# Performance work log

Hardware: AMD Instinct MI355X
Metric: run time of the kernel (lower is better)

The kernel has to match this reference:

```python
import jax, jax.numpy as jnp
import numpy as np

CAP = 512  # per-expert capacity; mean tokens/expert = 4096*4/64 = 256, CAP = mean + ~16 sigma (no drops for seed 0)


def _moe_forward(hidden_states, gate_w, w13, w2, top_k):
    T, H = hidden_states.shape
    E = gate_w.shape[0]
    # --- gating: softmax over expert logits, then top-k (npu_moe_gating_top_k_softmax) ---
    logits = hidden_states @ gate_w.T                      # [T, E]
    probs = jax.nn.softmax(logits, axis=-1)
    topk_w, topk_idx = jax.lax.top_k(probs, top_k)         # [T, K]
    # norm_topk_prob=True and top_k > 1
    topk_w = topk_w / (topk_w.sum(axis=-1, keepdims=True) + 1e-20)
    # --- init_routing: compute each (token, slot)'s rank within its expert ---
    N = T * top_k
    flat_e = topk_idx.reshape(N)                           # [N] expert id per expanded row
    order = jnp.argsort(flat_e)                            # stable sort by expert
    sorted_e = flat_e[order]
    counts = jax.ops.segment_sum(jnp.ones((N,), jnp.int32), flat_e, num_segments=E)
    starts = jnp.cumsum(counts) - counts                   # [E] start offset of each expert group
    rank_sorted = jnp.arange(N, dtype=jnp.int32) - starts[sorted_e].astype(jnp.int32)
    rank = jnp.zeros((N,), jnp.int32).at[order].set(rank_sorted)  # within-expert position
    # --- dispatch into [E, CAP, H] buffers (token gather/scatter) ---
    x_rep = jnp.repeat(hidden_states, top_k, axis=0)       # [N, H]
    disp = jnp.zeros((E, CAP, H), hidden_states.dtype).at[flat_e, rank].set(x_rep)
    # --- grouped GEMM: SwiGLU expert FFN as batched matmuls ---
    h = jnp.einsum('ech,ehf->ecf', disp, w13)              # [E, CAP, 2I]
    g, u = jnp.split(h, 2, axis=-1)
    a = jax.nn.silu(g) * u                                 # [E, CAP, I]
    y = jnp.einsum('eci,eih->ech', a, w2)                  # [E, CAP, H]
    # --- finalize_routing: gather back and weighted combine ---
    out_rows = y[flat_e, rank]                             # [N, H]
    out = (out_rows.reshape(T, top_k, H) * topk_w[..., None]).sum(axis=1)
    return out


def setup_inputs() -> dict:
    key = jax.random.key(0)
    k1, k2, k3, k4 = jax.random.split(key, 4)
    T, H, E, I = 4096, 2048, 64, 768
    hidden_states = jax.random.normal(k1, (T, H), dtype=jnp.float32)
    gate_w = jax.random.normal(k2, (E, H), dtype=jnp.float32) * 0.02
    w13 = jax.random.normal(k3, (E, H, 2 * I), dtype=jnp.float32) * 0.02
    w2 = jax.random.normal(k4, (E, I, H), dtype=jnp.float32) * 0.02
    return {"hidden_states": hidden_states, "gate_w": gate_w, "w13": w13, "w2": w2, "top_k": 4}


def reference(hidden_states, gate_w, w13, w2, top_k):
    return _moe_forward(hidden_states, gate_w, w13, w2, top_k)
```

## Files before the change

### kernel.cpp

```cpp
#include <hip/hip_runtime.h>
#include <hip/hip_bf16.h>

#define T_TOK 4096
#define HDIM  2048
#define NEXP  64
#define IDIM  768
#define TOPK  4
#define CAPE  512
#define NFLAT (T_TOK*TOPK)

typedef __bf16        bf16x8 __attribute__((ext_vector_type(8)));
typedef float         f32x4  __attribute__((ext_vector_type(4)));
typedef unsigned int  u32x4  __attribute__((ext_vector_type(4)));

__device__ __forceinline__ unsigned short f2bf(float f) {
  __bf16 b = (__bf16)f;
  return __builtin_bit_cast(unsigned short, b);
}
__device__ __forceinline__ unsigned pack2(float lo, float hi) {
  return (unsigned)f2bf(lo) | ((unsigned)f2bf(hi) << 16);
}
__device__ __forceinline__ int fswz(int row) { return ((row & 7) ^ ((row >> 3) & 7)) & 7; }
__device__ __forceinline__ int swz(int row, int chunk) {
  return row*128 + (((chunk ^ fswz(row)) & 7) << 4);
}
__device__ __forceinline__ void gload_lds16(const void* g, void* l) {
  __builtin_amdgcn_global_load_lds(
      (const __attribute__((address_space(1))) unsigned int*)g,
      (__attribute__((address_space(3))) unsigned int*)l, 16, 0, 0);
}

__global__ __launch_bounds__(256) void k_gating(
    const float* __restrict__ hs, const float* __restrict__ gw,
    unsigned short* __restrict__ hs_bf, int* __restrict__ tidx, float* __restrict__ tw)
{
  __shared__ float lg[16][64];
  const int tid = threadIdx.x;
  const int t0  = blockIdx.x * 16;

  {
    const f32x4* src = (const f32x4*)(hs + (size_t)t0 * HDIM);
    for (int i = tid; i < 16 * HDIM / 4; i += 256) {
      f32x4 v = src[i];
      ushort4 o;
      o.x = f2bf(v[0]); o.y = f2bf(v[1]); o.z = f2bf(v[2]); o.w = f2bf(v[3]);
      *(ushort4*)(hs_bf + (size_t)t0 * HDIM + (size_t)i * 4) = o;
    }
  }

  const int lane = tid & 63, wv = tid >> 6;
  {
    const f32x4* gr = (const f32x4*)(gw + (size_t)lane * HDIM);
    const f32x4* x0 = (const f32x4*)(hs + (size_t)(t0 + wv*4 + 0) * HDIM);
    const f32x4* x1 = (const f32x4*)(hs + (size_t)(t0 + wv*4 + 1) * HDIM);
    const f32x4* x2 = (const f32x4*)(hs + (size_t)(t0 + wv*4 + 2) * HDIM);
    const f32x4* x3 = (const f32x4*)(hs + (size_t)(t0 + wv*4 + 3) * HDIM);
    float a0=0.f, a1=0.f, a2=0.f, a3=0.f;
    for (int h = 0; h < HDIM/4; ++h) {
      f32x4 g = gr[h];
      f32x4 v0 = x0[h], v1 = x1[h], v2 = x2[h], v3 = x3[h];
      a0 += g[0]*v0[0] + g[1]*v0[1] + g[2]*v0[2] + g[3]*v0[3];
      a1 += g[0]*v1[0] + g[1]*v1[1] + g[2]*v1[2] + g[3]*v1[3];
      a2 += g[0]*v2[0] + g[1]*v2[1] + g[2]*v2[2] + g[3]*v2[3];
      a3 += g[0]*v3[0] + g[1]*v3[1] + g[2]*v3[2] + g[3]*v3[3];
    }
    lg[wv*4+0][lane] = a0;
    lg[wv*4+1][lane] = a1;
    lg[wv*4+2][lane] = a2;
    lg[wv*4+3][lane] = a3;
  }
  __syncthreads();

  if (tid < 16) {
    const int t = t0 + tid;
    unsigned long long chosen = 0ull;
    float bv[4]; int bi[4];
#pragma unroll
    for (int k = 0; k < 4; ++k) {
      float best = -1e30f; int b = 0;
      for (int e = 0; e < 64; ++e) {
        float v = lg[tid][e];
        if (!((chosen >> e) & 1ull) && v > best) { best = v; b = e; }
      }
      chosen |= 1ull << b; bv[k] = best; bi[k] = b;
    }
    float s = 0.f, w[4];
#pragma unroll
    for (int k = 0; k < 4; ++k) { w[k] = __expf(bv[k] - bv[0]); s += w[k]; }
    float inv = 1.f / s;
#pragma unroll
    for (int k = 0; k < 4; ++k) { tidx[t*4+k] = bi[k]; tw[t*4+k] = w[k] * inv; }
  }
}

__global__ __launch_bounds__(64) void k_count_rank(
    const int* __restrict__ tidx, int* __restrict__ rankb, int* __restrict__ counts)
{
  const int e = blockIdx.x;
  const int lane = threadIdx.x;
  int base = 0;
  for (int c = 0; c < NFLAT/64; ++c) {
    int n = c*64 + lane;
    bool m = (tidx[n] == e);
    unsigned long long mask = __ballot(m);
    if (m) rankb[n] = base + __popcll(mask & ((1ull << lane) - 1ull));
    base += __popcll(mask);
  }
  if (lane == 0) counts[e] = base;
}

__global__ __launch_bounds__(256) void k_build(
    const int* __restrict__ tidx, const int* __restrict__ rankb,
    const int* __restrict__ counts,
    int* __restrict__ starts, int* __restrict__ row_info, int* __restrict__ sortpos)
{
  __shared__ int s_starts[NEXP];
  if (threadIdx.x == 0) {
    int s = 0;
    for (int e = 0; e < NEXP; ++e) { s_starts[e] = s; starts[e] = s; s += counts[e]; }
  }
  __syncthreads();
  for (int n = threadIdx.x; n < NFLAT; n += 256) {
    int e = tidx[n], r = rankb[n];
    int sr = s_starts[e] + r;
    row_info[sr] = n;
    sortpos[n] = (r < CAPE) ? sr : -1;
  }
}

__global__ __launch_bounds__(512, 1) void k_gemm1(
    const unsigned short* __restrict__ hs_bf, const float* __restrict__ w13,
    const int* __restrict__ counts, const int* __restrict__ starts,
    const int* __restrict__ row_info, unsigned short* __restrict__ a_buf)
{
  const int b = blockIdx.x;
  const int e  = b / 12;
  const int nt = b % 12;
  const int count = min(counts[e], CAPE);
  if (count <= 0) return;
  const int nmt = (count + 255) >> 8;
  const int tid = threadIdx.x;
  const int estart = starts[e];
  const int NK = HDIM/64;

  __shared__ __align__(16) char lds[147456];

  const int lane = tid & 63, wv = tid >> 6;
  const int wr = wv >> 1, wc = wv & 1;

  int srcch[4];
#pragma unroll
  for (int r = 0; r < 4; ++r)
    srcch[r] = (lane & 7) ^ (lane >> 3) ^ ((wv*4 + r) & 7);

  const int n4 = (lane & 31) * 4;
  const int gcol = (n4 < 64) ? (nt*64 + n4) : (IDIM + nt*64 + (n4 - 64));
  const float* w13e = w13 + (size_t)e * HDIM * (2*IDIM) + gcol;

  const int pn = tid >> 2;
  const int ps = (tid & 3) * 2;

  for (int mit = 0; mit < nmt; ++mit) {
    const int R0 = mit << 8;
    const int base_sorted = estart + R0;
    int tokp[4];
#pragma unroll
    for (int r = 0; r < 4; ++r) {
      int sr = base_sorted + wv*32 + r*8 + (lane >> 3);
      if (sr > NFLAT-1) sr = NFLAT-1;
      tokp[r] = row_info[sr] >> 2;
    }

    f32x4 accg[4][2], accu[4][2];
#pragma unroll
    for (int i = 0; i < 4; ++i)
#pragma unroll
      for (int j = 0; j < 2; ++j) { accg[i][j] = f32x4{0.f,0.f,0.f,0.f}; accu[i][j] = f32x4{0.f,0.f,0.f,0.f}; }

    auto STAGE = [&](int p, int kt) {
      char* Al = lds + p*32768;
      char* Rl = lds + 65536 + p*32768;
#pragma unroll
      for (int r = 0; r < 4; ++r)
        gload_lds16(hs_bf + (size_t)tokp[r]*HDIM + kt*64 + srcch[r]*8,
                    Al + wv*4096 + r*1024 + lane*16);
#pragma unroll
      for (int r = 0; r < 4; ++r)
        gload_lds16(w13e + (size_t)(kt*64 + wv*8 + r*2 + (lane>>5)) * (2*IDIM),
                    Rl + (wv*8 + r*2 + (lane>>5))*512 + (lane & 31)*16);
    };

    STAGE(0, 0);
    for (int kt = 0; kt < NK; ++kt) {
      const int p = kt & 1;
      if (kt+1 < NK) {
        STAGE(p^1, kt+1);
        asm volatile("s_waitcnt vmcnt(8)" ::: "memory");
      } else {
        asm volatile("s_waitcnt vmcnt(0)" ::: "memory");
      }
      __builtin_amdgcn_s_barrier();

      {
        const char* Rl = lds + 65536 + p*32768;
        char* Bpk = lds + 131072;
        float pf[16];
#pragma unroll
        for (int j = 0; j < 16; ++j)
          pf[j] = *(const float*)(Rl + (ps*8 + j)*512 + pn*4);
        u32x4 q0, q1;
        q0[0] = pack2(pf[0],pf[1]);  q0[1] = pack2(pf[2],pf[3]);
        q0[2] = pack2(pf[4],pf[5]);  q0[3] = pack2(pf[6],pf[7]);
        q1[0] = pack2(pf[8],pf[9]);  q1[1] = pack2(pf[10],pf[11]);
        q1[2] = pack2(pf[12],pf[13]); q1[3] = pack2(pf[14],pf[15]);
        *(u32x4*)(Bpk + swz(pn, ps))   = q0;
        *(u32x4*)(Bpk + swz(pn, ps+1)) = q1;
      }
      bf16x8 af[2][4];
      {
        const char* Al = lds + p*32768;
#pragma unroll
        for (int kfi = 0; kfi < 2; ++kfi)
#pragma unroll
          for (int m2 = 0; m2 < 4; ++m2)
            af[kfi][m2] = *(const bf16x8*)(Al + swz(wr*64 + m2*16 + (lane & 15), (kfi<<2)|(lane>>4)));
      }
      asm volatile("s_waitcnt lgkmcnt(0)" ::: "memory");
      __builtin_amdgcn_s_barrier();

      const char* Bpk = lds + 131072;
#pragma unroll
      for (int kfi = 0; kfi < 2; ++kfi) {
        const int ch = (kfi<<2) | (lane>>4);
        bf16x8 bg[2], bu[2];
#pragma unroll
        for (int ni = 0; ni < 2; ++ni) {
          int ic = wc*32 + ni*16 + (lane & 15);
          bg[ni] = *(const bf16x8*)(Bpk + swz(ic, ch));
          bu[ni] = *(const bf16x8*)(Bpk + swz(64 + ic, ch));
        }
#pragma unroll
        for (int m2 = 0; m2 < 4; ++m2)
#pragma unroll
          for (int ni = 0; ni < 2; ++ni) {
            accg[m2][ni] = __builtin_amdgcn_mfma_f32_16x16x32_bf16(af[kfi][m2], bg[ni], accg[m2][ni], 0, 0, 0);
            accu[m2][ni] = __builtin_amdgcn_mfma_f32_16x16x32_bf16(af[kfi][m2], bu[ni], accu[m2][ni], 0, 0, 0);
          }
      }
    }

#pragma unroll
    for (int m2 = 0; m2 < 4; ++m2) {
#pragma unroll
      for (int j = 0; j < 4; ++j) {
        int rl = wr*64 + m2*16 + (lane >> 4)*4 + j;
        if (R0 + rl < count) {
          size_t rowoff = (size_t)(base_sorted + rl) * IDIM;
#pragma unroll
          for (int ni = 0; ni < 2; ++ni) {
            int col = nt*64 + wc*32 + ni*16 + (lane & 15);
            float g = accg[m2][ni][j], u = accu[m2][ni][j];
            float a = (g / (1.f + __expf(-g))) * u;
            a_buf[rowoff + col] = f2bf(a);
          }
        }
      }
    }
  }
}

__global__ __launch_bounds__(512, 1) void k_gemm2(
    const unsigned short* __restrict__ a_buf, const float* __restrict__ w2,
    const int* __restrict__ counts, const int* __restrict__ starts,
    unsigned short* __restrict__ y_buf)
{
  const int b = blockIdx.x;
  const int e  = b >> 4;
  const int nt = b & 15;
  const int count = min(counts[e], CAPE);
  if (count <= 0) return;
  const int nmt = (count + 255) >> 8;
  const int tid = threadIdx.x;
  const int estart = starts[e];
  const int NK = IDIM/64;

  __shared__ __align__(16) char lds[147456];

  const int lane = tid & 63, wv = tid >> 6;
  const int wr = wv >> 1, wc = wv & 1;

  int srcch[4];
#pragma unroll
  for (int r = 0; r < 4; ++r)
    srcch[r] = (lane & 7) ^ (lane >> 3) ^ ((wv*4 + r) & 7);

  const int n4 = (lane & 31) * 4;
  const float* w2e = w2 + (size_t)e * IDIM * HDIM + (size_t)nt*128 + n4;

  const int pn = tid >> 2;
  const int ps = (tid & 3) * 2;

  for (int mit = 0; mit < nmt; ++mit) {
    const int R0 = mit << 8;
    const int base_sorted = estart + R0;
    int srp[4];
#pragma unroll
    for (int r = 0; r < 4; ++r) {
      int sr = base_sorted + wv*32 + r*8 + (lane >> 3);
      srp[r] = (sr > NFLAT-1) ? (NFLAT-1) : sr;
    }

    f32x4 acc[4][4];
#pragma unroll
    for (int i = 0; i < 4; ++i)
#pragma unroll
      for (int j = 0; j < 4; ++j) acc[i][j] = f32x4{0.f,0.f,0.f,0.f};

    auto STAGE = [&](int p, int kt) {
      char* Al = lds + p*32768;
      char* Rl = lds + 65536 + p*32768;
#pragma unroll
      for (int r = 0; r < 4; ++r)
        gload_lds16(a_buf + (size_t)srp[r]*IDIM + kt*64 + srcch[r]*8,
                    Al + wv*4096 + r*1024 + lane*16);
#pragma unroll
      for (int r = 0; r < 4; ++r)
        gload_lds16(w2e + (size_t)(kt*64 + wv*8 + r*2 + (lane>>5)) * HDIM,
                    Rl + (wv*8 + r*2 + (lane>>5))*512 + (lane & 31)*16);
    };

    STAGE(0, 0);
    for (int kt = 0; kt < NK; ++kt) {
      const int p = kt & 1;
      if (kt+1 < NK) {
        STAGE(p^1, kt+1);
        asm volatile("s_waitcnt vmcnt(8)" ::: "memory");
      } else {
        asm volatile("s_waitcnt vmcnt(0)" ::: "memory");
      }
      __builtin_amdgcn_s_barrier();

      {
        const char* Rl = lds + 65536 + p*32768;
        char* Bpk = lds + 131072;
        float pf[16];
#pragma unroll
        for (int j = 0; j < 16; ++j)
          pf[j] = *(const float*)(Rl + (ps*8 + j)*512 + pn*4);
        u32x4 q0, q1;
        q0[0] = pack2(pf[0],pf[1]);  q0[1] = pack2(pf[2],pf[3]);
        q0[2] = pack2(pf[4],pf[5]);  q0[3] = pack2(pf[6],pf[7]);
        q1[0] = pack2(pf[8],pf[9]);  q1[1] = pack2(pf[10],pf[11]);
        q1[2] = pack2(pf[12],pf[13]); q1[3] = pack2(pf[14],pf[15]);
        *(u32x4*)(Bpk + swz(pn, ps))   = q0;
        *(u32x4*)(Bpk + swz(pn, ps+1)) = q1;
      }
      bf16x8 af[2][4];
      {
        const char* Al = lds + p*32768;
#pragma unroll
        for (int kfi = 0; kfi < 2; ++kfi)
#pragma unroll
          for (int m2 = 0; m2 < 4; ++m2)
            af[kfi][m2] = *(const bf16x8*)(Al + swz(wr*64 + m2*16 + (lane & 15), (kfi<<2)|(lane>>4)));
      }
      asm volatile("s_waitcnt lgkmcnt(0)" ::: "memory");
      __builtin_amdgcn_s_barrier();

      const char* Bpk = lds + 131072;
#pragma unroll
      for (int kfi = 0; kfi < 2; ++kfi) {
        const int ch = (kfi<<2) | (lane>>4);
        bf16x8 bb[4];
#pragma unroll
        for (int ni = 0; ni < 4; ++ni)
          bb[ni] = *(const bf16x8*)(Bpk + swz(wc*64 + ni*16 + (lane & 15), ch));
#pragma unroll
        for (int m2 = 0; m2 < 4; ++m2)
#pragma unroll
          for (int ni = 0; ni < 4; ++ni)
            acc[m2][ni] = __builtin_amdgcn_mfma_f32_16x16x32_bf16(af[kfi][m2], bb[ni], acc[m2][ni], 0, 0, 0);
      }
    }

#pragma unroll
    for (int m2 = 0; m2 < 4; ++m2) {
#pragma unroll
      for (int j = 0; j < 4; ++j) {
        int rl = wr*64 + m2*16 + (lane >> 4)*4 + j;
        if (R0 + rl < count) {
          int sr = base_sorted + rl;
          unsigned short* yrow = y_buf + (size_t)sr * HDIM;
#pragma unroll
          for (int ni = 0; ni < 4; ++ni) {
            int col = nt*128 + wc*64 + ni*16 + (lane & 15);
            yrow[col] = f2bf(acc[m2][ni][j]);
          }
        }
      }
    }
  }
}

__global__ __launch_bounds__(256) void k_finalize(
    const unsigned short* __restrict__ y_buf, const int* __restrict__ sortpos,
    const float* __restrict__ tw, float* __restrict__ out)
{
  const int t = blockIdx.x;
  const int tid = threadIdx.x;
  float acc[8];
#pragma unroll
  for (int i = 0; i < 8; ++i) acc[i] = 0.f;
#pragma unroll
  for (int k = 0; k < 4; ++k) {
    int sp = sortpos[t*4+k];
    float w = tw[t*4+k];
    if (sp >= 0) {
      u32x4 v = *(const u32x4*)(y_buf + (size_t)sp * HDIM + tid*8);
#pragma unroll
      for (int q = 0; q < 4; ++q) {
        float lo = __builtin_bit_cast(float, v[q] << 16);
        float hi = __builtin_bit_cast(float, v[q] & 0xffff0000u);
        acc[2*q]   += w * lo;
        acc[2*q+1] += w * hi;
      }
    }
  }
  f32x4 o0 = {acc[0], acc[1], acc[2], acc[3]};
  f32x4 o1 = {acc[4], acc[5], acc[6], acc[7]};
  f32x4* o = (f32x4*)(out + (size_t)t * HDIM + tid*8);
  o[0] = o0;
  o[1] = o1;
}

extern "C" void kernel_launch(void* const* d_in, const int* in_sizes, int n_in,
                              void* d_out, int out_size, void* d_ws, size_t ws_size,
                              hipStream_t stream) {
  const float* hs  = (const float*)d_in[0];
  const float* gw  = (const float*)d_in[1];
  const float* w13 = (const float*)d_in[2];
  const float* w2  = (const float*)d_in[3];
  float* out = (float*)d_out;

  char* ws = (char*)d_ws;
  size_t off = 0;
  auto alloc = [&](size_t bytes) {
    off = (off + 255) & ~(size_t)255;
    char* p = ws + off;
    off += bytes;
    return p;
  };
  unsigned short* hs_bf = (unsigned short*)alloc((size_t)T_TOK * HDIM * 2);
  int*   tidx   = (int*)  alloc((size_t)NFLAT * 4);
  float* tw     = (float*)alloc((size_t)NFLAT * 4);
  int*   rankb  = (int*)  alloc((size_t)NFLAT * 4);
  int*   counts = (int*)  alloc((size_t)NEXP * 4);
  int*   starts = (int*)  alloc((size_t)NEXP * 4);
  int*   rinfo  = (int*)  alloc((size_t)NFLAT * 4);
  int*   sortp  = (int*)  alloc((size_t)NFLAT * 4);
  unsigned short* a_buf = (unsigned short*)alloc((size_t)NFLAT * IDIM * 2);
  unsigned short* y_buf = (unsigned short*)alloc((size_t)NFLAT * HDIM * 2);
  (void)ws_size; (void)in_sizes; (void)n_in; (void)out_size;

  k_gating<<<T_TOK/16, 256, 0, stream>>>(hs, gw, hs_bf, tidx, tw);
  k_count_rank<<<NEXP, 64, 0, stream>>>(tidx, rankb, counts);
  k_build<<<1, 256, 0, stream>>>(tidx, rankb, counts, starts, rinfo, sortp);
  k_gemm1<<<dim3(12*NEXP), 512, 0, stream>>>(hs_bf, w13, counts, starts, rinfo, a_buf);
  k_gemm2<<<dim3(16*NEXP), 512, 0, stream>>>(a_buf, w2, counts, starts, y_buf);
  k_finalize<<<T_TOK, 256, 0, stream>>>(y_buf, sortp, tw, out);
}
```

Before: 843.2 us.

## Shrink GEMM LDS footprint and drop double buffering to raise occupancy

```diff
diff --git a/kernel.cpp b/kernel.cpp
--- a/kernel.cpp
+++ b/kernel.cpp
@@ -128,7 +128,7 @@
   }
 }
 
-__global__ __launch_bounds__(512, 1) void k_gemm1(
+__global__ __launch_bounds__(512, 4) void k_gemm1(
     const unsigned short* __restrict__ hs_bf, const float* __restrict__ w13,
     const int* __restrict__ counts, const int* __restrict__ starts,
     const int* __restrict__ row_info, unsigned short* __restrict__ a_buf)
@@ -143,22 +143,24 @@
   const int estart = starts[e];
   const int NK = HDIM/64;
 
-  __shared__ __align__(16) char lds[147456];
+  __shared__ __align__(16) char lds[81920];
 
   const int lane = tid & 63, wv = tid >> 6;
-  const int wr = wv >> 1, wc = wv & 1;
+  const int wr = wv >> 2, wc = wv & 3;
 
   int srcch[4];
 #pragma unroll
-  for (int r = 0; r < 4; ++r)
-    srcch[r] = (lane & 7) ^ (lane >> 3) ^ ((wv*4 + r) & 7);
-
+  for (int r = 0; r < 4; ++r) {
+    int row = r*64 + wv*8 + (lane >> 3);
+    srcch[r] = ((lane & 7) ^ fswz(row)) & 7;
+  }
   const int n4 = (lane & 31) * 4;
   const int gcol = (n4 < 64) ? (nt*64 + n4) : (IDIM + nt*64 + (n4 - 64));
-  const float* w13e = w13 + (size_t)e * HDIM * (2*IDIM) + gcol;
-
-  const int pn = tid >> 2;
-  const int ps = (tid & 3) * 2;
+  const float* w13base = w13 + (size_t)e * HDIM * (2*IDIM) + gcol;
+  const int kofs = wv*2 + (lane >> 5);
+
+  const int pn = tid & 127;
+  const int ps = (tid >> 7) * 2;
 
   for (int mit = 0; mit < nmt; ++mit) {
     const int R0 = mit << 8;
@@ -166,110 +168,80 @@
     int tokp[4];
 #pragma unroll
     for (int r = 0; r < 4; ++r) {
-      int sr = base_sorted + wv*32 + r*8 + (lane >> 3);
+      int sr = base_sorted + r*64 + wv*8 + (lane >> 3);
       if (sr > NFLAT-1) sr = NFLAT-1;
       tokp[r] = row_info[sr] >> 2;
     }
 
-    f32x4 accg[4][2], accu[4][2];
-#pragma unroll
-    for (int i = 0; i < 4; ++i)
-#pragma unroll
-      for (int j = 0; j < 2; ++j) { accg[i][j] = f32x4{0.f,0.f,0.f,0.f}; accu[i][j] = f32x4{0.f,0.f,0.f,0.f}; }
-
-    auto STAGE = [&](int p, int kt) {
-      char* Al = lds + p*32768;
-      char* Rl = lds + 65536 + p*32768;
+    f32x4 accg[8], accu[8];
+#pragma unroll
+    for (int i = 0; i < 8; ++i) { accg[i] = f32x4{0.f,0.f,0.f,0.f}; accu[i] = f32x4{0.f,0.f,0.f,0.f}; }
+
+    for (int kt = 0; kt < NK; ++kt) {
 #pragma unroll
       for (int r = 0; r < 4; ++r)
         gload_lds16(hs_bf + (size_t)tokp[r]*HDIM + kt*64 + srcch[r]*8,
-                    Al + wv*4096 + r*1024 + lane*16);
+                    lds + r*8192 + wv*1024 + lane*16);
 #pragma unroll
       for (int r = 0; r < 4; ++r)
-        gload_lds16(w13e + (size_t)(kt*64 + wv*8 + r*2 + (lane>>5)) * (2*IDIM),
-                    Rl + (wv*8 + r*2 + (lane>>5))*512 + (lane & 31)*16);
-    };
-
-    STAGE(0, 0);
-    for (int kt = 0; kt < NK; ++kt) {
-      const int p = kt & 1;
-      if (kt+1 < NK) {
-        STAGE(p^1, kt+1);
-        asm volatile("s_waitcnt vmcnt(8)" ::: "memory");
-      } else {
-        asm volatile("s_waitcnt vmcnt(0)" ::: "memory");
-      }
-      __builtin_amdgcn_s_barrier();
+        gload_lds16(w13base + (size_t)(kt*64 + r*16 + kofs) * (2*IDIM),
+                    lds + 32768 + r*8192 + wv*1024 + lane*16);
+      __syncthreads();
 
       {
-        const char* Rl = lds + 65536 + p*32768;
-        char* Bpk = lds + 131072;
         float pf[16];
 #pragma unroll
         for (int j = 0; j < 16; ++j)
-          pf[j] = *(const float*)(Rl + (ps*8 + j)*512 + pn*4);
+          pf[j] = *(const float*)(lds + 32768 + (ps*8 + j)*512 + pn*4);
         u32x4 q0, q1;
-        q0[0] = pack2(pf[0],pf[1]);  q0[1] = pack2(pf[2],pf[3]);
-        q0[2] = pack2(pf[4],pf[5]);  q0[3] = pack2(pf[6],pf[7]);
-        q1[0] = pack2(pf[8],pf[9]);  q1[1] = pack2(pf[10],pf[11]);
+        q0[0] = pack2(pf[0],pf[1]);   q0[1] = pack2(pf[2],pf[3]);
+        q0[2] = pack2(pf[4],pf[5]);   q0[3] = pack2(pf[6],pf[7]);
+        q1[0] = pack2(pf[8],pf[9]);   q1[1] = pack2(pf[10],pf[11]);
         q1[2] = pack2(pf[12],pf[13]); q1[3] = pack2(pf[14],pf[15]);
-        *(u32x4*)(Bpk + swz(pn, ps))   = q0;
-        *(u32x4*)(Bpk + swz(pn, ps+1)) = q1;
-      }
-      bf16x8 af[2][4];
-      {
-        const char* Al = lds + p*32768;
-#pragma unroll
-        for (int kfi = 0; kfi < 2; ++kfi)
-#pragma unroll
-          for (int m2 = 0; m2 < 4; ++m2)
-            af[kfi][m2] = *(const bf16x8*)(Al + swz(wr*64 + m2*16 + (lane & 15), (kfi<<2)|(lane>>4)));
-      }
-      asm volatile("s_waitcnt lgkmcnt(0)" ::: "memory");
-      __builtin_amdgcn_s_barrier();
-
-      const char* Bpk = lds + 131072;
+        *(u32x4*)(lds + 65536 + swz(pn, ps))   = q0;
+        *(u32x4*)(lds + 65536 + swz(pn, ps+1)) = q1;
+      }
+      bf16x8 af[2][8];
+#pragma unroll
+      for (int kfi = 0; kfi < 2; ++kfi)
+#pragma unroll
+        for (int m2 = 0; m2 < 8; ++m2)
+          af[kfi][m2] = *(const bf16x8*)(lds + swz(wr*128 + m2*16 + (lane & 15), (kfi<<2)|(lane>>4)));
+      __syncthreads();
+
 #pragma unroll
       for (int kfi = 0; kfi < 2; ++kfi) {
         const int ch = (kfi<<2) | (lane>>4);
-        bf16x8 bg[2], bu[2];
-#pragma unroll
-        for (int ni = 0; ni < 2; ++ni) {
-          int ic = wc*32 + ni*16 + (lane & 15);
-          bg[ni] = *(const bf16x8*)(Bpk + swz(ic, ch));
-          bu[ni] = *(const bf16x8*)(Bpk + swz(64 + ic, ch));
+        const int ic = wc*16 + (lane & 15);
+        bf16x8 bg = *(const bf16x8*)(lds + 65536 + swz(ic, ch));
+        bf16x8 bu = *(const bf16x8*)(lds + 65536 + swz(64 + ic, ch));
+#pragma unroll
+        for (int m2 = 0; m2 < 8; ++m2) {
+          accg[m2] = __builtin_amdgcn_mfma_f32_16x16x32_bf16(af[kfi][m2], bg, accg[m2], 0, 0, 0);
+          accu[m2] = __builtin_amdgcn_mfma_f32_16x16x32_bf16(af[kfi][m2], bu, accu[m2], 0, 0, 0);
         }
-#pragma unroll
-        for (int m2 = 0; m2 < 4; ++m2)
-#pragma unroll
-          for (int ni = 0; ni < 2; ++ni) {
-            accg[m2][ni] = __builtin_amdgcn_mfma_f32_16x16x32_bf16(af[kfi][m2], bg[ni], accg[m2][ni], 0, 0, 0);
-            accu[m2][ni] = __builtin_amdgcn_mfma_f32_16x16x32_bf16(af[kfi][m2], bu[ni], accu[m2][ni], 0, 0, 0);
-          }
-      }
-    }
-
-#pragma unroll
-    for (int m2 = 0; m2 < 4; ++m2) {
+      }
+    }
+
+#pragma unroll
+    for (int m2 = 0; m2 < 8; ++m2) {
 #pragma unroll
       for (int j = 0; j < 4; ++j) {
-        int rl = wr*64 + m2*16 + (lane >> 4)*4 + j;
+        int rl = wr*128 + m2*16 + (lane >> 4)*4 + j;
         if (R0 + rl < count) {
           size_t rowoff = (size_t)(base_sorted + rl) * IDIM;
-#pragma unroll
-          for (int ni = 0; ni < 2; ++ni) {
-            int col = nt*64 + wc*32 + ni*16 + (lane & 15);
-            float g = accg[m2][ni][j], u = accu[m2][ni][j];
-            float a = (g / (1.f + __expf(-g))) * u;
-            a_buf[rowoff + col] = f2bf(a);
-          }
+          int col = nt*64 + wc*16 + (lane & 15);
+          float g = accg[m2][j], u = accu[m2][j];
+          float a = (g / (1.f + __expf(-g))) * u;
+          a_buf[rowoff + col] = f2bf(a);
         }
       }
     }
-  }
-}
-
-__global__ __launch_bounds__(512, 1) void k_gemm2(
+    __syncthreads();
+  }
+}
+
+__global__ __launch_bounds__(512, 4) void k_gemm2(
     const unsigned short* __restrict__ a_buf, const float* __restrict__ w2,
     const int* __restrict__ counts, const int* __restrict__ starts,
     unsigned short* __restrict__ y_buf)
@@ -284,21 +256,23 @@
   const int estart = starts[e];
   const int NK = IDIM/64;
 
-  __shared__ __align__(16) char lds[147456];
+  __shared__ __align__(16) char lds[81920];
 
   const int lane = tid & 63, wv = tid >> 6;
-  const int wr = wv >> 1, wc = wv & 1;
+  const int wr = wv >> 2, wc = wv & 3;
 
   int srcch[4];
 #pragma unroll
-  for (int r = 0; r < 4; ++r)
-    srcch[r] = (lane & 7) ^ (lane >> 3) ^ ((wv*4 + r) & 7);
-
+  for (int r = 0; r < 4; ++r) {
+    int row = r*64 + wv*8 + (lane >> 3);
+    srcch[r] = ((lane & 7) ^ fswz(row)) & 7;
+  }
   const int n4 = (lane & 31) * 4;
-  const float* w2e = w2 + (size_t)e * IDIM * HDIM + (size_t)nt*128 + n4;
-
-  const int pn = tid >> 2;
-  const int ps = (tid & 3) * 2;
+  const float* w2base = w2 + (size_t)e * IDIM * HDIM + (size_t)nt*128 + n4;
+  const int kofs = wv*2 + (lane >> 5);
+
+  const int pn = tid & 127;
+  const int ps = (tid >> 7) * 2;
 
   for (int mit = 0; mit < nmt; ++mit) {
     const int R0 = mit << 8;
@@ -306,99 +280,80 @@
     int srp[4];
 #pragma unroll
     for (int r = 0; r < 4; ++r) {
-      int sr = base_sorted + wv*32 + r*8 + (lane >> 3);
+      int sr = base_sorted + r*64 + wv*8 + (lane >> 3);
       srp[r] = (sr > NFLAT-1) ? (NFLAT-1) : sr;
     }
 
-    f32x4 acc[4][4];
-#pragma unroll
-    for (int i = 0; i < 4; ++i)
-#pragma unroll
-      for (int j = 0; j < 4; ++j) acc[i][j] = f32x4{0.f,0.f,0.f,0.f};
-
-    auto STAGE = [&](int p, int kt) {
-      char* Al = lds + p*32768;
-      char* Rl = lds + 65536 + p*32768;
+    f32x4 acc[8][2];
+#pragma unroll
+    for (int i = 0; i < 8; ++i)
+#pragma unroll
+      for (int j = 0; j < 2; ++j) acc[i][j] = f32x4{0.f,0.f,0.f,0.f};
+
+    for (int kt = 0; kt < NK; ++kt) {
 #pragma unroll
       for (int r = 0; r < 4; ++r)
         gload_lds16(a_buf + (size_t)srp[r]*IDIM + kt*64 + srcch[r]*8,
-                    Al + wv*4096 + r*1024 + lane*16);
+                    lds + r*8192 + wv*1024 + lane*16);
 #pragma unroll
       for (int r = 0; r < 4; ++r)
-        gload_lds16(w2e + (size_t)(kt*64 + wv*8 + r*2 + (lane>>5)) * HDIM,
-                    Rl + (wv*8 + r*2 + (lane>>5))*512 + (lane & 31)*16);
-    };
-
-    STAGE(0, 0);
-    for (int kt = 0; kt < NK; ++kt) {
-      const int p = kt & 1;
-      if (kt+1 < NK) {
-        STAGE(p^1, kt+1);
-        asm volatile("s_waitcnt vmcnt(8)" ::: "memory");
-      } else {
-        asm volatile("s_waitcnt vmcnt(0)" ::: "memory");
-      }
-      __builtin_amdgcn_s_barrier();
+        gload_lds16(w2base + (size_t)(kt*64 + r*16 + kofs) * HDIM,
+                    lds + 32768 + r*8192 + wv*1024 + lane*16);
+      __syncthreads();
 
       {
-        const char* Rl = lds + 65536 + p*32768;
-        char* Bpk = lds + 131072;
         float pf[16];
 #pragma unroll
         for (int j = 0; j < 16; ++j)
-          pf[j] = *(const float*)(Rl + (ps*8 + j)*512 + pn*4);
+          pf[j] = *(const float*)(lds + 32768 + (ps*8 + j)*512 + pn*4);
         u32x4 q0, q1;
-        q0[0] = pack2(pf[0],pf[1]);  q0[1] = pack2(pf[2],pf[3]);
-        q0[2] = pack2(pf[4],pf[5]);  q0[3] = pack2(pf[6],pf[7]);
-        q1[0] = pack2(pf[8],pf[9]);  q1[1] = pack2(pf[10],pf[11]);
+        q0[0] = pack2(pf[0],pf[1]);   q0[1] = pack2(pf[2],pf[3]);
+        q0[2] = pack2(pf[4],pf[5]);   q0[3] = pack2(pf[6],pf[7]);
+        q1[0] = pack2(pf[8],pf[9]);   q1[1] = pack2(pf[10],pf[11]);
         q1[2] = pack2(pf[12],pf[13]); q1[3] = pack2(pf[14],pf[15]);
-        *(u32x4*)(Bpk + swz(pn, ps))   = q0;
-        *(u32x4*)(Bpk + swz(pn, ps+1)) = q1;
-      }
-      bf16x8 af[2][4];
-      {
-        const char* Al = lds + p*32768;
-#pragma unroll
-        for (int kfi = 0; kfi < 2; ++kfi)
-#pragma unroll
-          for (int m2 = 0; m2 < 4; ++m2)
-            af[kfi][m2] = *(const bf16x8*)(Al + swz(wr*64 + m2*16 + (lane & 15), (kfi<<2)|(lane>>4)));
-      }
-      asm volatile("s_waitcnt lgkmcnt(0)" ::: "memory");
-      __builtin_amdgcn_s_barrier();
-
-      const char* Bpk = lds + 131072;
+        *(u32x4*)(lds + 65536 + swz(pn, ps))   = q0;
+        *(u32x4*)(lds + 65536 + swz(pn, ps+1)) = q1;
+      }
+      bf16x8 af[2][8];
+#pragma unroll
+      for (int kfi = 0; kfi < 2; ++kfi)
+#pragma unroll
+        for (int m2 = 0; m2 < 8; ++m2)
+          af[kfi][m2] = *(const bf16x8*)(lds + swz(wr*128 + m2*16 + (lane & 15), (kfi<<2)|(lane>>4)));
+      __syncthreads();
+
 #pragma unroll
       for (int kfi = 0; kfi < 2; ++kfi) {
         const int ch = (kfi<<2) | (lane>>4);
-        bf16x8 bb[4];
-#pragma unroll
-        for (int ni = 0; ni < 4; ++ni)
-          bb[ni] = *(const bf16x8*)(Bpk + swz(wc*64 + ni*16 + (lane & 15), ch));
-#pragma unroll
-        for (int m2 = 0; m2 < 4; ++m2)
-#pragma unroll
-          for (int ni = 0; ni < 4; ++ni)
+        bf16x8 bb[2];
+#pragma unroll
+        for (int ni = 0; ni < 2; ++ni)
+          bb[ni] = *(const bf16x8*)(lds + 65536 + swz(wc*32 + ni*16 + (lane & 15), ch));
+#pragma unroll
+        for (int m2 = 0; m2 < 8; ++m2)
+#pragma unroll
+          for (int ni = 0; ni < 2; ++ni)
             acc[m2][ni] = __builtin_amdgcn_mfma_f32_16x16x32_bf16(af[kfi][m2], bb[ni], acc[m2][ni], 0, 0, 0);
       }
     }
 
 #pragma unroll
-    for (int m2 = 0; m2 < 4; ++m2) {
+    for (int m2 = 0; m2 < 8; ++m2) {
 #pragma unroll
       for (int j = 0; j < 4; ++j) {
-        int rl = wr*64 + m2*16 + (lane >> 4)*4 + j;
+        int rl = wr*128 + m2*16 + (lane >> 4)*4 + j;
         if (R0 + rl < count) {
           int sr = base_sorted + rl;
           unsigned short* yrow = y_buf + (size_t)sr * HDIM;
 #pragma unroll
-          for (int ni = 0; ni < 4; ++ni) {
-            int col = nt*128 + wc*64 + ni*16 + (lane & 15);
+          for (int ni = 0; ni < 2; ++ni) {
+            int col = nt*128 + wc*32 + ni*16 + (lane & 15);
             yrow[col] = f2bf(acc[m2][ni][j]);
           }
         }
       }
     }
+    __syncthreads();
   }
 }
 
```

After: 2.485 ms. 2.95x slower.
